# Kernel optimization log

Measured on AMD Instinct MI355X. Metric: run time of the kernel, lower is better.

## Reference

```python
import jax, jax.numpy as jnp
import numpy as np

D_MODEL = 1024
D_STATE = 8          # max(8, 16 // 2)
D_CONV = 4
D_INNER = int(1.5 * D_MODEL)   # expand = max(1.5, 2*0.75)
DT_RANK = (D_MODEL + 15) // 16 # 64
D_FF = 2 * D_MODEL
B, L = 2, 2048


def layer_norm(x, g, b, eps=1e-5):
    mu = jnp.mean(x, -1, keepdims=True)
    var = jnp.var(x, -1, keepdims=True)
    return (x - mu) * jax.lax.rsqrt(var + eps) * g + b


def setup_inputs() -> dict:
    key = jax.random.key(0)
    ks = jax.random.split(key, 12)
    def n(k, shape, scale=0.02):
        return jax.random.normal(k, shape, dtype=jnp.float32) * scale
    return {
        'x': jax.random.normal(ks[0], (B, L, D_MODEL), dtype=jnp.float32),
        'ln1_g': jnp.ones((D_MODEL,), jnp.float32),
        'ln1_b': jnp.zeros((D_MODEL,), jnp.float32),
        'ln2_g': jnp.ones((D_MODEL,), jnp.float32),
        'ln2_b': jnp.zeros((D_MODEL,), jnp.float32),
        'in_proj_w': n(ks[1], (2 * D_INNER, D_MODEL)),
        'conv_w': n(ks[2], (D_INNER, 1, D_CONV), 0.1),
        'conv_b': jnp.zeros((D_INNER,), jnp.float32),
        'x_proj_w': n(ks[3], (DT_RANK + 2 * D_STATE, D_INNER)),
        'dt_proj_w': n(ks[4], (D_INNER, DT_RANK), 0.1),
        'dt_proj_b': n(ks[5], (D_INNER,), 0.1),
        'A_log': jnp.log(jnp.broadcast_to(jnp.arange(1, D_STATE + 1, dtype=jnp.float32), (D_INNER, D_STATE))),
        'D': jnp.ones((D_INNER,), jnp.float32),
        'out_proj_w': n(ks[6], (D_MODEL, D_INNER)),
        'ffn_w1': n(ks[7], (D_FF, D_MODEL)),
        'ffn_b1': jnp.zeros((D_FF,), jnp.float32),
        'ffn_w2': n(ks[8], (D_MODEL, D_FF)),
        'ffn_b2': jnp.zeros((D_MODEL,), jnp.float32),
    }


def mamba(x, in_proj_w, conv_w, conv_b, x_proj_w, dt_proj_w, dt_proj_b, A_log, Dp, out_proj_w):
    # in_proj -> (x, z)
    xz = x @ in_proj_w.T                       # (B, L, 2*d_inner)
    xi, z = jnp.split(xz, 2, axis=-1)
    # depthwise causal conv over seq, kernel 4
    xc = jnp.transpose(xi, (0, 2, 1))          # (B, d_inner, L)
    xc = jax.lax.conv_general_dilated(
        xc, conv_w, window_strides=(1,), padding=[(D_CONV - 1, 0)],
        dimension_numbers=('NCH', 'OIH', 'NCH'), feature_group_count=D_INNER)
    xc = xc + conv_b[None, :, None]
    u = jax.nn.silu(jnp.transpose(xc, (0, 2, 1)))  # (B, L, d_inner)
    # x_proj -> dt, B, C
    x_dbl = u @ x_proj_w.T
    dt = x_dbl[..., :DT_RANK]
    Bm = x_dbl[..., DT_RANK:DT_RANK + D_STATE]
    Cm = x_dbl[..., DT_RANK + D_STATE:]
    delta = jax.nn.softplus(dt @ dt_proj_w.T + dt_proj_b)  # (B, L, d_inner)
    A = -jnp.exp(A_log)                                    # (d_inner, d_state)
    dA = jnp.exp(jnp.einsum('bld,dn->bldn', delta, A))     # (B, L, d_inner, d_state)
    dBu = jnp.einsum('bld,bln,bld->bldn', delta, Bm, u)
    # selective scan over time
    def step(h, inputs):
        dA_t, dBu_t, C_t = inputs
        h = dA_t * h + dBu_t                   # (B, d_inner, d_state)
        y = jnp.einsum('bdn,bn->bd', h, C_t)
        return h, y
    h0 = jnp.zeros((x.shape[0], D_INNER, D_STATE), x.dtype)
    _, ys = jax.lax.scan(step, h0, (jnp.moveaxis(dA, 1, 0), jnp.moveaxis(dBu, 1, 0), jnp.moveaxis(Cm, 1, 0)))
    y = jnp.moveaxis(ys, 0, 1) + u * Dp        # skip connection D*u
    y = y * jax.nn.silu(z)                     # gate
    return y @ out_proj_w.T


def reference(x, ln1_g, ln1_b, ln2_g, ln2_b, in_proj_w, conv_w, conv_b, x_proj_w,
              dt_proj_w, dt_proj_b, A_log, D, out_proj_w, ffn_w1, ffn_b1, ffn_w2, ffn_b2):
    residual = x
    xp = layer_norm(x, ln1_g, ln1_b)
    x = mamba(xp, in_proj_w, conv_w, conv_b, x_proj_w, dt_proj_w, dt_proj_b, A_log, D, out_proj_w) + residual
    xn = layer_norm(x, ln2_g, ln2_b)
    h = jax.nn.gelu(xn @ ffn_w1.T + ffn_b1, approximate=False)  # dropout is identity in eval
    return x + (h @ ffn_w2.T + ffn_b2)
```

## Files before the change

### kernel.cpp

```cpp
#include <hip/hip_runtime.h>
#include <math.h>

#define D_MODEL 1024
#define D_STATE 8
#define D_CONV  4
#define D_INNER 1536
#define DT_RANK 64
#define D_FF    2048
#define BATCH   2
#define SEQ     2048
#define NROWS   (BATCH*SEQ)
#define NC      32
#define LC      (SEQ/NC)
#define XPAD    128

typedef short bf16x8 __attribute__((ext_vector_type(8)));
typedef unsigned short u16x8 __attribute__((ext_vector_type(8)));
typedef float f32x4  __attribute__((ext_vector_type(4)));

__device__ inline unsigned short f2bf(float x) {
    union { float f; unsigned u; } v; v.f = x;
    unsigned r = v.u + 0x7fffu + ((v.u >> 16) & 1u);
    return (unsigned short)(r >> 16);
}
__device__ inline float bf2f(unsigned short h) {
    union { unsigned u; float f; } v; v.u = ((unsigned)h) << 16;
    return v.f;
}
__device__ inline float softplus_f(float x) {
    return (x > 20.0f) ? x : log1pf(__expf(x));
}
__device__ inline float gelu_f(float x) {
    return 0.5f * x * (1.0f + erff(x * 0.70710678118654752f));
}
__device__ inline float silu_f(float x) {
    return x / (1.0f + __expf(-x));
}
__device__ inline void gload16(const unsigned short* g, unsigned short* l) {
    typedef unsigned int u32;
    __builtin_amdgcn_global_load_lds(
        (const __attribute__((address_space(1))) u32*)g,
        (__attribute__((address_space(3))) u32*)l, 16, 0, 0);
}

#define PHASE_SYNC_PRE()  do { __builtin_amdgcn_s_barrier(); \
                               asm volatile("s_waitcnt lgkmcnt(0)" ::: "memory"); } while (0)
#define PHASE_SYNC_POST() do { __builtin_amdgcn_s_barrier(); } while (0)

__global__ __launch_bounds__(256) void prep_kernel(
    const float* __restrict__ s0, unsigned short* __restrict__ d0,
    const float* __restrict__ s1, unsigned short* __restrict__ d1,
    const float* __restrict__ s2, unsigned short* __restrict__ d2,
    const float* __restrict__ s3, unsigned short* __restrict__ d3,
    const float* __restrict__ s4, unsigned short* __restrict__ d4,
    const float* __restrict__ xpw, unsigned short* __restrict__ xpd,
    const float* __restrict__ x, const float* __restrict__ g1,
    const float* __restrict__ b1, unsigned short* __restrict__ xout) {
    int b = blockIdx.x;
    if (b < 4400) {
        const float* s; unsigned short* d; int base;
        if      (b < 1536) { s = s0; d = d0; base = b * 2048; }
        else if (b < 1584) { s = s1; d = d1; base = (b - 1536) * 2048; }
        else if (b < 2352) { s = s2; d = d2; base = (b - 1584) * 2048; }
        else if (b < 3376) { s = s3; d = d3; base = (b - 2352) * 2048; }
        else               { s = s4; d = d4; base = (b - 3376) * 2048; }
        int i = base + threadIdx.x * 8;
        float4 v0 = *(const float4*)(s + i);
        float4 v1 = *(const float4*)(s + i + 4);
        ushort4 a, c;
        a.x = f2bf(v0.x); a.y = f2bf(v0.y); a.z = f2bf(v0.z); a.w = f2bf(v0.w);
        c.x = f2bf(v1.x); c.y = f2bf(v1.y); c.z = f2bf(v1.z); c.w = f2bf(v1.w);
        *(ushort4*)(d + i)     = a;
        *(ushort4*)(d + i + 4) = c;
    } else if (b < 4528) {
        int row = b - 4400;
        for (int c = threadIdx.x; c < D_INNER; c += 256)
            xpd[row * D_INNER + c] = (row < 80) ? f2bf(xpw[row * D_INNER + c]) : (unsigned short)0;
    } else {
        __shared__ float sbuf[4];
        int row = b - 4528;
        int t = threadIdx.x;
        float4 v = ((const float4*)(x + (size_t)row * D_MODEL))[t];
        float s = v.x + v.y + v.z + v.w;
        for (int o = 32; o; o >>= 1) s += __shfl_down(s, o, 64);
        if ((t & 63) == 0) sbuf[t >> 6] = s;
        __syncthreads();
        float mu = (sbuf[0] + sbuf[1] + sbuf[2] + sbuf[3]) * (1.0f / D_MODEL);
        __syncthreads();
        float e0 = v.x - mu, e1 = v.y - mu, e2 = v.z - mu, e3 = v.w - mu;
        float q = e0*e0 + e1*e1 + e2*e2 + e3*e3;
        for (int o = 32; o; o >>= 1) q += __shfl_down(q, o, 64);
        if ((t & 63) == 0) sbuf[t >> 6] = q;
        __syncthreads();
        float var = (sbuf[0] + sbuf[1] + sbuf[2] + sbuf[3]) * (1.0f / D_MODEL);
        float rs = rsqrtf(var + 1e-5f);
        float4 gv = ((const float4*)g1)[t];
        float4 bv = ((const float4*)b1)[t];
        ushort4 st;
        st.x = f2bf(e0 * rs * gv.x + bv.x);
        st.y = f2bf(e1 * rs * gv.y + bv.y);
        st.z = f2bf(e2 * rs * gv.z + bv.z);
        st.w = f2bf(e3 * rs * gv.w + bv.w);
        ((ushort4*)(xout + (size_t)row * D_MODEL))[t] = st;
    }
}

__global__ __launch_bounds__(256) void ln_kernel(const float* __restrict__ x,
                                                 const float* __restrict__ g,
                                                 const float* __restrict__ b,
                                                 unsigned short* __restrict__ out) {
    __shared__ float sbuf[4];
    int row = blockIdx.x;
    int t = threadIdx.x;
    float4 v = ((const float4*)(x + (size_t)row * D_MODEL))[t];
    float s = v.x + v.y + v.z + v.w;
    for (int o = 32; o; o >>= 1) s += __shfl_down(s, o, 64);
    if ((t & 63) == 0) sbuf[t >> 6] = s;
    __syncthreads();
    float mu = (sbuf[0] + sbuf[1] + sbuf[2] + sbuf[3]) * (1.0f / D_MODEL);
    __syncthreads();
    float d0 = v.x - mu, d1 = v.y - mu, d2 = v.z - mu, d3 = v.w - mu;
    float q = d0*d0 + d1*d1 + d2*d2 + d3*d3;
    for (int o = 32; o; o >>= 1) q += __shfl_down(q, o, 64);
    if ((t & 63) == 0) sbuf[t >> 6] = q;
    __syncthreads();
    float var = (sbuf[0] + sbuf[1] + sbuf[2] + sbuf[3]) * (1.0f / D_MODEL);
    float rs = rsqrtf(var + 1e-5f);
    float4 gv = ((const float4*)g)[t];
    float4 bv = ((const float4*)b)[t];
    ushort4 st;
    st.x = f2bf(d0 * rs * gv.x + bv.x);
    st.y = f2bf(d1 * rs * gv.y + bv.y);
    st.z = f2bf(d2 * rs * gv.z + bv.z);
    st.w = f2bf(d3 * rs * gv.w + bv.w);
    ((ushort4*)(out + (size_t)row * D_MODEL))[t] = st;
}

#define EPI_F32        0
#define EPI_F32_BF16   1
#define EPI_SOFTPLUS   2
#define EPI_RESID      3
#define EPI_GELU_BF16  4
#define EPI_BIAS_RESID 5
#define EPI_BF16       6
#define EPI_SOFTPLUS_BF16 7

template<int WN, int EPI, int SPLITK>
__global__ __launch_bounds__(512, 2) void gemm8p(
    const unsigned short* __restrict__ A, int lda,
    const unsigned short* __restrict__ Bm, int ldb, int K,
    float* __restrict__ Cf, unsigned short* __restrict__ Cb, int ldc,
    const float* __restrict__ bias,
    const float* __restrict__ resid, int ldr) {
    constexpr int WM = 8 / WN;
    constexpr int BN = WN * 64;
    constexpr int RW = 256 / WM;
    constexpr int CW = 64;
    constexpr int MI = RW / 16;
    constexpr int NI = CW / 16;
    constexpr int MIH = MI / 2, NIH = NI / 2;
    constexpr int ABYTES = 256 * 128;
    constexpr int BBYTES = BN * 128;
    constexpr int BOFF = 2 * ABYTES;
    __shared__ unsigned short lds[(2 * ABYTES + 2 * BBYTES) / 2];

    const int t = threadIdx.x, l = t & 63, w = t >> 6;
    const int wr = w / WN, wc = w % WN;

    const int nx = gridDim.x;
    const int nwg = nx * gridDim.y;
    int bid = blockIdx.y * nx + blockIdx.x;
    int q = nwg >> 3;
    int swz = (bid & 7) * q + (bid >> 3);
    const int m0 = (swz / nx) * 256, n0 = (swz % nx) * BN;
    const int kbase = (SPLITK > 1) ? blockIdx.z * K : 0;

    const int sr = l >> 3;
    const int sj = ((l & 7) * 16) ^ ((l >> 3) << 4);
    const int row_l = w * 8;
    const int row_c = (w >> 2) * 64 + (w & 3) * 8;

    auto STG = [&](int bufbyte, int rowbase, const unsigned short* G, int ldg, int gbase, int kt) {
        unsigned short* dst = (unsigned short*)((char*)lds + bufbyte + rowbase * 128);
        const unsigned short* src = G + (size_t)(gbase + rowbase + sr) * ldg + kbase + kt * 64 + (sj >> 1);
        gload16(src, dst);
    };
    auto S_Ah0 = [&](int b, int kt) {
        if (WN == 4) { STG(b * ABYTES, row_l, A, lda, m0, kt);       STG(b * ABYTES, 128 + row_l, A, lda, m0, kt); }
        else         { STG(b * ABYTES, row_c, A, lda, m0, kt);       STG(b * ABYTES, 128 + row_c, A, lda, m0, kt); }
    };
    auto S_Ah1 = [&](int b, int kt) {
        if (WN == 4) { STG(b * ABYTES, 64 + row_l, A, lda, m0, kt);  STG(b * ABYTES, 192 + row_l, A, lda, m0, kt); }
        else         { STG(b * ABYTES, 32 + row_c, A, lda, m0, kt);  STG(b * ABYTES, 160 + row_c, A, lda, m0, kt); }
    };
    auto S_Bc0 = [&](int b, int kt) {
        if (WN == 4) { STG(BOFF + b * BBYTES, row_c, Bm, ldb, n0, kt); STG(BOFF + b * BBYTES, 128 + row_c, Bm, ldb, n0, kt); }
        else         { STG(BOFF + b * BBYTES, row_c, Bm, ldb, n0, kt); }
    };
    auto S_Bc1 = [&](int b, int kt) {
        if (WN == 4) { STG(BOFF + b * BBYTES, 32 + row_c, Bm, ldb, n0, kt); STG(BOFF + b * BBYTES, 160 + row_c, Bm, ldb, n0, kt); }
        else         { STG(BOFF + b * BBYTES, 32 + row_c, Bm, ldb, n0, kt); }
    };

    auto LD = [&](int bytebase, int row, int kb) -> bf16x8 {
        int o = bytebase + row * 128 + (kb ^ ((row & 7) << 4));
        return *(const bf16x8*)((const char*)lds + o);
    };

    f32x4 acc[MI][NI] = {};
    bf16x8 af[MIH][2], b0v[NIH][2], b1v[NIH][2];

    auto LDA_set = [&](int buf, int qr, auto& dst) {
        #pragma unroll
        for (int mi = 0; mi < MIH; mi++)
            #pragma unroll
            for (int ks = 0; ks < 2; ks++)
                dst[mi][ks] = LD(buf * ABYTES, wr * RW + qr * (RW / 2) + mi * 16 + (l & 15),
                                 ks * 64 + (l >> 4) * 16);
    };
    auto LDB_set = [&](int buf, int qc, auto& dst) {
        #pragma unroll
        for (int ni2 = 0; ni2 < NIH; ni2++)
            #pragma unroll
            for (int ks = 0; ks < 2; ks++)
                dst[ni2][ks] = LD(BOFF + buf * BBYTES, wc * CW + qc * 32 + ni2 * 16 + (l & 15),
                                  ks * 64 + (l >> 4) * 16);
    };
    auto MFMA_Q = [&](int qr, int qc, auto& a_, auto& b_) {
        __builtin_amdgcn_s_setprio(1);
        #pragma unroll
        for (int mi = 0; mi < MIH; mi++)
            #pragma unroll
            for (int ni2 = 0; ni2 < NIH; ni2++)
                #pragma unroll
                for (int ks = 0; ks < 2; ks++)
                    acc[qr * MIH + mi][qc * NIH + ni2] =
                        __builtin_amdgcn_mfma_f32_16x16x32_bf16(a_[mi][ks], b_[ni2][ks],
                                                                acc[qr * MIH + mi][qc * NIH + ni2], 0, 0, 0);
        __builtin_amdgcn_s_setprio(0);
    };
    auto VMW = [&](bool last) {
        if (last)            asm volatile("s_waitcnt vmcnt(0)" ::: "memory");
        else if (WN == 4)    asm volatile("s_waitcnt vmcnt(6)" ::: "memory");
        else                 asm volatile("s_waitcnt vmcnt(5)" ::: "memory");
    };

    const int ni_ = K >> 7;

    S_Ah0(0, 0); S_Ah1(0, 0); S_Bc0(0, 0); S_Bc1(0, 0);
    S_Ah0(1, 1); S_Ah1(1, 1); S_Bc0(1, 1); S_Bc1(1, 1);
    if (WN == 4) asm volatile("s_waitcnt vmcnt(8)" ::: "memory");
    else         asm volatile("s_waitcnt vmcnt(6)" ::: "memory");
    __builtin_amdgcn_s_barrier();

    for (int i = 0; i < ni_; i++) {
        const bool last = (i == ni_ - 1);
        const int t2 = 2 * i + 2, t3 = 2 * i + 3;
        LDA_set(0, 0, af); LDB_set(0, 0, b0v);
        if (i) S_Bc0(1, 2 * i + 1);
        PHASE_SYNC_PRE(); MFMA_Q(0, 0, af, b0v); PHASE_SYNC_POST();
        LDB_set(0, 1, b1v);
        if (!last) S_Ah0(0, t2);
        PHASE_SYNC_PRE(); MFMA_Q(0, 1, af, b1v); PHASE_SYNC_POST();
        LDA_set(0, 1, af);
        PHASE_SYNC_PRE(); MFMA_Q(1, 1, af, b1v); PHASE_SYNC_POST();
        LDB_set(0, 0, b0v);
        if (!last) { S_Ah1(0, t2); S_Bc1(0, t2); }
        VMW(last);
        PHASE_SYNC_PRE(); MFMA_Q(1, 0, af, b0v); PHASE_SYNC_POST();
        LDA_set(1, 0, af); LDB_set(1, 0, b0v);
        if (!last) S_Bc0(0, t2);
        PHASE_SYNC_PRE(); MFMA_Q(0, 0, af, b0v); PHASE_SYNC_POST();
        LDB_set(1, 1, b1v);
        if (!last) S_Ah0(1, t3);
        PHASE_SYNC_PRE(); MFMA_Q(0, 1, af, b1v); PHASE_SYNC_POST();
        LDA_set(1, 1, af);
        PHASE_SYNC_PRE(); MFMA_Q(1, 1, af, b1v); PHASE_SYNC_POST();
        LDB_set(1, 0, b0v);
        if (!last) { S_Ah1(1, t3); S_Bc1(1, t3); }
        VMW(last);
        PHASE_SYNC_PRE(); MFMA_Q(1, 0, af, b0v); PHASE_SYNC_POST();
    }

    float* Cfp = Cf;
    if (SPLITK > 1) Cfp += (size_t)blockIdx.z * NROWS * ldc;
    #pragma unroll
    for (int ni2 = 0; ni2 < NI; ni2++) {
        int col = n0 + wc * CW + ni2 * 16 + (l & 15);
        float bv = 0.0f;
        if (EPI == EPI_SOFTPLUS || EPI == EPI_GELU_BF16 || EPI == EPI_BIAS_RESID) bv = bias[col];
        #pragma unroll
        for (int mi = 0; mi < MI; mi++) {
            #pragma unroll
            for (int j = 0; j < 4; j++) {
                int row = m0 + wr * RW + mi * 16 + (l >> 4) * 4 + j;
                float v = acc[mi][ni2][j];
                if (EPI == EPI_SOFTPLUS)        v = softplus_f(v + bv);
                else if (EPI == EPI_GELU_BF16)  v = gelu_f(v + bv);
                else if (EPI == EPI_RESID)      v = v + resid[(size_t)row * ldr + col];
                else if (EPI == EPI_BIAS_RESID) v = v + bv + resid[(size_t)row * ldr + col];
                if (EPI == EPI_GELU_BF16 || EPI == EPI_BF16) {
                    Cb[(size_t)row * ldc + col] = f2bf(v);
                } else {
                    Cfp[(size_t)row * ldc + col] = v;
                    if (EPI == EPI_F32_BF16) Cb[(size_t)row * ldc + col] = f2bf(v);
                }
            }
        }
    }
}

__global__ __launch_bounds__(256) void sk2_ln(const float* __restrict__ p,
                                              const float* __restrict__ resid,
                                              const float* __restrict__ g,
                                              const float* __restrict__ b,
                                              float* __restrict__ x2,
                                              unsigned short* __restrict__ xn) {
    __shared__ float sbuf[4];
    int row = blockIdx.x;
    int t = threadIdx.x;
    const size_t seg = (size_t)NROWS * D_MODEL;
    size_t base = (size_t)row * D_MODEL + t * 4;
    float4 a = *(const float4*)(p + base);
    float4 bb = *(const float4*)(p + base + seg);
    float4 r = *(const float4*)(resid + base);
    float4 v;
    v.x = a.x + bb.x + r.x;
    v.y = a.y + bb.y + r.y;
    v.z = a.z + bb.z + r.z;
    v.w = a.w + bb.w + r.w;
    *(float4*)(x2 + base) = v;
    float s = v.x + v.y + v.z + v.w;
    for (int o = 32; o; o >>= 1) s += __shfl_down(s, o, 64);
    if ((t & 63) == 0) sbuf[t >> 6] = s;
    __syncthreads();
    float mu = (sbuf[0] + sbuf[1] + sbuf[2] + sbuf[3]) * (1.0f / D_MODEL);
    __syncthreads();
    float d0 = v.x - mu, d1 = v.y - mu, d2 = v.z - mu, d3 = v.w - mu;
    float qq = d0*d0 + d1*d1 + d2*d2 + d3*d3;
    for (int o = 32; o; o >>= 1) qq += __shfl_down(qq, o, 64);
    if ((t & 63) == 0) sbuf[t >> 6] = qq;
    __syncthreads();
    float var = (sbuf[0] + sbuf[1] + sbuf[2] + sbuf[3]) * (1.0f / D_MODEL);
    float rs = rsqrtf(var + 1e-5f);
    float4 gv = ((const float4*)g)[t];
    float4 bv = ((const float4*)b)[t];
    ushort4 st;
    st.x = f2bf(d0 * rs * gv.x + bv.x);
    st.y = f2bf(d1 * rs * gv.y + bv.y);
    st.z = f2bf(d2 * rs * gv.z + bv.z);
    st.w = f2bf(d3 * rs * gv.w + bv.w);
    ((ushort4*)(xn + (size_t)row * D_MODEL))[t] = st;
}

__global__ __launch_bounds__(256) void sk2_reduce(const float* __restrict__ p,
                                                  const float* __restrict__ bias,
                                                  const float* __restrict__ resid,
                                                  float* __restrict__ o) {
    int i = (blockIdx.x * 256 + threadIdx.x) * 4;
    const size_t seg = (size_t)NROWS * D_MODEL;
    float4 a = *(const float4*)(p + i);
    float4 b = *(const float4*)(p + i + seg);
    float4 r = *(const float4*)(resid + i);
    float4 bb = *(const float4*)(bias + (i & (D_MODEL - 1)));
    float4 o4;
    o4.x = a.x + b.x + r.x + bb.x;
    o4.y = a.y + b.y + r.y + bb.y;
    o4.z = a.z + b.z + r.z + bb.z;
    o4.w = a.w + b.w + r.w + bb.w;
    *(float4*)(o + i) = o4;
}

template<int EPI, int SPLITK>
__global__ __launch_bounds__(256) void gemm_mfma(
    const unsigned short* __restrict__ A, int lda,
    const unsigned short* __restrict__ B, int ldb, int K,
    float* __restrict__ Cf, unsigned short* __restrict__ Cb, int ldc,
    const float* __restrict__ bias,
    const float* __restrict__ resid, int ldr) {
    __shared__ unsigned short As[3][128 * 32];
    __shared__ unsigned short Bs[3][128 * 32];
    int t = threadIdx.x, l = t & 63, w = t >> 6;
    int nx = gridDim.x;
    int nwg = nx * gridDim.y;
    int bid = blockIdx.y * nx + blockIdx.x;
    int q = nwg >> 3;
    int swz = (bid & 7) * q + (bid >> 3);
    int m0 = (swz / nx) * 128, n0 = (swz % nx) * 128;
    int kbase = (SPLITK > 1) ? blockIdx.z * K : 0;
    int c0 = 2 * w, c1 = 2 * w + 1;
    int srow = l >> 2, scol = (l & 3) * 8;
    const unsigned short* Ag0 = A + (size_t)(m0 + 16 * c0 + srow) * lda + kbase + scol;
    const unsigned short* Ag1 = A + (size_t)(m0 + 16 * c1 + srow) * lda + kbase + scol;
    const unsigned short* Bg0 = B + (size_t)(n0 + 16 * c0 + srow) * ldb + kbase + scol;
    const unsigned short* Bg1 = B + (size_t)(n0 + 16 * c1 + srow) * ldb + kbase + scol;
    int wr = w >> 1, wc = w & 1;
    int aoff = (wr * 64 + (l & 15)) * 32 + (l >> 4) * 8;
    int boff = (wc * 64 + (l & 15)) * 32 + (l >> 4) * 8;

    f32x4 acc[4][4] = {};
    int nt = K >> 5;

    gload16(Ag0, &As[0][c0 * 512]);
    gload16(Ag1, &As[0][c1 * 512]);
    gload16(Bg0, &Bs[0][c0 * 512]);
    gload16(Bg1, &Bs[0][c1 * 512]);
    if (nt > 1) {
        gload16(Ag0 + 32, &As[1][c0 * 512]);
        gload16(Ag1 + 32, &As[1][c1 * 512]);
        gload16(Bg0 + 32, &Bs[1][c0 * 512]);
        gload16(Bg1 + 32, &Bs[1][c1 * 512]);
    }

    int cur = 0;
    for (int ti = 0; ti < nt; ti++) {
        int pf = ti + 2;
        if (pf < nt) {
            int nb = cur - 1; if (nb < 0) nb += 3;
            int k0 = pf << 5;
            gload16(Ag0 + k0, &As[nb][c0 * 512]);
            gload16(Ag1 + k0, &As[nb][c1 * 512]);
            gload16(Bg0 + k0, &Bs[nb][c0 * 512]);
            gload16(Bg1 + k0, &Bs[nb][c1 * 512]);
        }
        int rem = nt - 1 - ti;
        if (rem >= 2)      asm volatile("s_waitcnt vmcnt(8)" ::: "memory");
        else if (rem == 1) asm volatile("s_waitcnt vmcnt(4)" ::: "memory");
        else               asm volatile("s_waitcnt vmcnt(0)" ::: "memory");
        __builtin_amdgcn_s_barrier();

        const unsigned short* Ab = &As[cur][0];
        const unsigned short* Bb = &Bs[cur][0];
        bf16x8 af[4], bfv[4];
        #pragma unroll
        for (int i = 0; i < 4; i++) af[i] = *(const bf16x8*)(Ab + aoff + i * 512);
        #pragma unroll
        for (int i = 0; i < 4; i++) bfv[i] = *(const bf16x8*)(Bb + boff + i * 512);
        __builtin_amdgcn_s_setprio(1);
        #pragma unroll
        for (int mi = 0; mi < 4; mi++)
            #pragma unroll
            for (int ni = 0; ni < 4; ni++)
                acc[mi][ni] = __builtin_amdgcn_mfma_f32_16x16x32_bf16(af[mi], bfv[ni], acc[mi][ni], 0, 0, 0);
        __builtin_amdgcn_s_setprio(0);
        __builtin_amdgcn_s_barrier();
        cur++; if (cur == 3) cur = 0;
    }

    if (SPLITK > 1) Cf += (size_t)blockIdx.z * NROWS * ldc;
    int colb = n0 + wc * 64 + (l & 15);
    int rowb = m0 + wr * 64 + (l >> 4) * 4;
    #pragma unroll
    for (int ni = 0; ni < 4; ni++) {
        int col = colb + ni * 16;
        float bv = 0.0f;
        if (EPI == EPI_SOFTPLUS || EPI == EPI_GELU_BF16 || EPI == EPI_BIAS_RESID || EPI == EPI_SOFTPLUS_BF16) bv = bias[col];
        #pragma unroll
        for (int mi = 0; mi < 4; mi++) {
            #pragma unroll
            for (int j = 0; j < 4; j++) {
                int row = rowb + mi * 16 + j;
                float v = acc[mi][ni][j];
                if (EPI == EPI_SOFTPLUS || EPI == EPI_SOFTPLUS_BF16) v = softplus_f(v + bv);
                else if (EPI == EPI_GELU_BF16)  v = gelu_f(v + bv);
                else if (EPI == EPI_RESID)      v = v + resid[(size_t)row * ldr + col];
                else if (EPI == EPI_BIAS_RESID) v = v + bv + resid[(size_t)row * ldr + col];
                if (EPI == EPI_GELU_BF16 || EPI == EPI_BF16 || EPI == EPI_SOFTPLUS_BF16) {
                    Cb[(size_t)row * ldc + col] = f2bf(v);
                } else {
                    Cf[(size_t)row * ldc + col] = v;
                    if (EPI == EPI_F32_BF16) Cb[(size_t)row * ldc + col] = f2bf(v);
                }
            }
        }
    }
}

__global__ __launch_bounds__(256) void xdbl_reduce(const float* __restrict__ part,
                                                   float* __restrict__ xdbl,
                                                   unsigned short* __restrict__ xdbl_bf) {
    int i = blockIdx.x * 256 + threadIdx.x;
    const size_t seg = (size_t)NROWS * XPAD;
    float s = part[i] + part[i + seg] + part[i + 2 * seg] + part[i + 3 * seg];
    xdbl[i] = s;
    xdbl_bf[i] = f2bf(s);
}

__global__ __launch_bounds__(256) void conv_silu(const unsigned short* __restrict__ xz,
                                                 const float* __restrict__ w,
                                                 const float* __restrict__ cb,
                                                 unsigned short* __restrict__ u) {
    int idx = (blockIdx.x * 256 + threadIdx.x) * 8;
    int d = idx % D_INNER;
    int bl = idx / D_INNER;
    int l = bl & (SEQ - 1);
    float acc[8];
    float4 wv[8];
    #pragma unroll
    for (int j = 0; j < 8; j++) wv[j] = *(const float4*)(w + (d + j) * 4);
    float4 cb0 = *(const float4*)(cb + d);
    float4 cb1 = *(const float4*)(cb + d + 4);
    acc[0] = cb0.x; acc[1] = cb0.y; acc[2] = cb0.z; acc[3] = cb0.w;
    acc[4] = cb1.x; acc[5] = cb1.y; acc[6] = cb1.z; acc[7] = cb1.w;
    #pragma unroll
    for (int k = 0; k < 4; k++) {
        int lp = l - 3 + k;
        if (lp >= 0) {
            u16x8 s = *(const u16x8*)(xz + (size_t)(bl - 3 + k) * (2 * D_INNER) + d);
            #pragma unroll
            for (int j = 0; j < 8; j++) {
                float wk = (k == 0) ? wv[j].x : (k == 1) ? wv[j].y : (k == 2) ? wv[j].z : wv[j].w;
                acc[j] += bf2f((unsigned short)s[j]) * wk;
            }
        }
    }
    u16x8 o;
    #pragma unroll
    for (int j = 0; j < 8; j++) o[j] = f2bf(silu_f(acc[j]));
    *(u16x8*)(u + idx) = o;
}

__global__ __launch_bounds__(256) void scan_passA(const unsigned short* __restrict__ delta,
                                                  const unsigned short* __restrict__ u,
                                                  const float* __restrict__ xdbl,
                                                  const float* __restrict__ A_log,
                                                  float* __restrict__ P,
                                                  float* __restrict__ S) {
    int d = blockIdx.x * 256 + threadIdx.x;
    int c = blockIdx.y, b = blockIdx.z;
    __shared__ float bc[LC][16];
    int base_row = b * SEQ + c * LC;
    for (int e = threadIdx.x; e < LC * 16; e += 256) {
        int lrr = e >> 4, col = e & 15;
        bc[lrr][col] = xdbl[(size_t)(base_row + lrr) * XPAD + DT_RANK + col];
    }
    __syncthreads();
    float Ad[8];
    #pragma unroll
    for (int n = 0; n < 8; n++) Ad[n] = -__expf(A_log[d * 8 + n]);
    float prod[8], hs[8];
    #pragma unroll
    for (int n = 0; n < 8; n++) { prod[n] = 1.0f; hs[n] = 0.0f; }
    for (int lrr = 0; lrr < LC; lrr++) {
        int row = base_row + lrr;
        float dl = bf2f(delta[(size_t)row * D_INNER + d]);
        float uu = bf2f(u[(size_t)row * D_INNER + d]);
        float du = dl * uu;
        #pragma unroll
        for (int n = 0; n < 8; n++) {
            float dA = __expf(dl * Ad[n]);
            prod[n] *= dA;
            hs[n] = dA * hs[n] + du * bc[lrr][n];
        }
    }
    size_t o = ((size_t)((size_t)b * NC + c) * D_INNER + d) * 8;
    #pragma unroll
    for (int n = 0; n < 8; n++) { P[o + n] = prod[n]; S[o + n] = hs[n]; }
}

__global__ __launch_bounds__(256) void scan_passB(const float* __restrict__ P,
                                                  const float* __restrict__ S,
                                                  float* __restrict__ hstart) {
    int tid = blockIdx.x * 256 + threadIdx.x;
    int b = tid / (D_INNER * 8);
    int rem = tid % (D_INNER * 8);
    float h = 0.0f;
    for (int c = 0; c < NC; c++) {
        size_t o = (size_t)(b * NC + c) * (D_INNER * 8) + rem;
        hstart[o] = h;
        h = P[o] * h + S[o];
    }
}

__global__ __launch_bounds__(256) void scan_passC(const unsigned short* __restrict__ delta,
                                                  const unsigned short* __restrict__ u,
                                                  const float* __restrict__ xdbl,
                                                  const float* __restrict__ A_log,
                                                  const float* __restrict__ hstart,
                                                  const unsigned short* __restrict__ xz,
                                                  const float* __restrict__ Dp,
                                                  unsigned short* __restrict__ ygate) {
    int d = blockIdx.x * 256 + threadIdx.x;
    int c = blockIdx.y, b = blockIdx.z;
    __shared__ float bc[LC][16];
    int base_row = b * SEQ + c * LC;
    for (int e = threadIdx.x; e < LC * 16; e += 256) {
        int lrr = e >> 4, col = e & 15;
        bc[lrr][col] = xdbl[(size_t)(base_row + lrr) * XPAD + DT_RANK + col];
    }
    __syncthreads();
    float Ad[8];
    #pragma unroll
    for (int n = 0; n < 8; n++) Ad[n] = -__expf(A_log[d * 8 + n]);
    float h[8];
    size_t ho = ((size_t)((size_t)b * NC + c) * D_INNER + d) * 8;
    #pragma unroll
    for (int n = 0; n < 8; n++) h[n] = hstart[ho + n];
    float Dd = Dp[d];
    for (int lrr = 0; lrr < LC; lrr++) {
        int row = base_row + lrr;
        float dl = bf2f(delta[(size_t)row * D_INNER + d]);
        float uu = bf2f(u[(size_t)row * D_INNER + d]);
        float du = dl * uu;
        float y = 0.0f;
        #pragma unroll
        for (int n = 0; n < 8; n++) {
            float dA = __expf(dl * Ad[n]);
            h[n] = dA * h[n] + du * bc[lrr][n];
            y += h[n] * bc[lrr][8 + n];
        }
        y += uu * Dd;
        float z = bf2f(xz[(size_t)row * (2 * D_INNER) + D_INNER + d]);
        ygate[(size_t)row * D_INNER + d] = f2bf(y * silu_f(z));
    }
}

extern "C" void kernel_launch(void* const* d_in, const int* in_sizes, int n_in,
                              void* d_out, int out_size, void* d_ws, size_t ws_size,
                              hipStream_t stream) {
    const float* x         = (const float*)d_in[0];
    const float* ln1_g     = (const float*)d_in[1];
    const float* ln1_b     = (const float*)d_in[2];
    const float* ln2_g     = (const float*)d_in[3];
    const float* ln2_b     = (const float*)d_in[4];
    const float* in_proj_w = (const float*)d_in[5];
    const float* conv_w    = (const float*)d_in[6];
    const float* conv_b    = (const float*)d_in[7];
    const float* x_proj_w  = (const float*)d_in[8];
    const float* dt_proj_w = (const float*)d_in[9];
    const float* dt_proj_b = (const float*)d_in[10];
    const float* A_log     = (const float*)d_in[11];
    const float* Dp        = (const float*)d_in[12];
    const float* out_proj_w= (const float*)d_in[13];
    const float* ffn_w1    = (const float*)d_in[14];
    const float* ffn_b1    = (const float*)d_in[15];
    const float* ffn_w2    = (const float*)d_in[16];
    const float* ffn_b2    = (const float*)d_in[17];
    float* out = (float*)d_out;

    float* xdbl  = (float*)d_ws;
    float* P     = xdbl + (size_t)NROWS * XPAD;
    float* S     = P + (size_t)BATCH * NC * D_INNER * 8;
    float* hst   = S + (size_t)BATCH * NC * D_INNER * 8;
    float* x2    = hst + (size_t)BATCH * NC * D_INNER * 8;
    float* psum  = x2 + (size_t)NROWS * D_MODEL;
    float* part  = psum;
    unsigned short* xz_bf   = (unsigned short*)(psum + 2 * (size_t)NROWS * D_MODEL);
    unsigned short* xp_bf   = xz_bf + (size_t)NROWS * 2 * D_INNER;
    unsigned short* u_bf    = xp_bf + (size_t)NROWS * D_MODEL;
    unsigned short* xdbl_bf = u_bf + (size_t)NROWS * D_INNER;
    unsigned short* yg_bf   = xdbl_bf + (size_t)NROWS * XPAD;
    unsigned short* dl_bf   = yg_bf + (size_t)NROWS * D_INNER;
    unsigned short* w_in    = dl_bf + (size_t)NROWS * D_INNER;
    unsigned short* w_xp    = w_in + (size_t)2 * D_INNER * D_MODEL;
    unsigned short* w_dt    = w_xp + (size_t)XPAD * D_INNER;
    unsigned short* w_out   = w_dt + (size_t)D_INNER * DT_RANK;
    unsigned short* w_f1    = w_out + (size_t)D_MODEL * D_INNER;
    unsigned short* w_f2    = w_f1 + (size_t)D_FF * D_MODEL;
    unsigned short* hff_bf  = xz_bf;

    prep_kernel<<<4400 + XPAD + NROWS, 256, 0, stream>>>(
        in_proj_w, w_in, dt_proj_w, w_dt, out_proj_w, w_out, ffn_w1, w_f1, ffn_w2, w_f2,
        x_proj_w, w_xp, x, ln1_g, ln1_b, xp_bf);
    gemm8p<4, EPI_BF16, 1><<<dim3(3072 / 256, NROWS / 256), 512, 0, stream>>>(
        xp_bf, D_MODEL, w_in, D_MODEL, D_MODEL, nullptr, xz_bf, 2 * D_INNER, nullptr, nullptr, 0);
    conv_silu<<<(NROWS * D_INNER) / (256 * 8), 256, 0, stream>>>(xz_bf, conv_w, conv_b, u_bf);
    gemm_mfma<EPI_F32, 4><<<dim3(1, NROWS / 128, 4), 256, 0, stream>>>(
        u_bf, D_INNER, w_xp, D_INNER, D_INNER / 4, part, nullptr, XPAD, nullptr, nullptr, 0);
    xdbl_reduce<<<(NROWS * XPAD) / 256, 256, 0, stream>>>(part, xdbl, xdbl_bf);
    gemm_mfma<EPI_SOFTPLUS_BF16, 1><<<dim3(D_INNER / 128, NROWS / 128), 256, 0, stream>>>(
        xdbl_bf, XPAD, w_dt, DT_RANK, DT_RANK, nullptr, dl_bf, D_INNER, dt_proj_b, nullptr, 0);
    scan_passA<<<dim3(D_INNER / 256, NC, BATCH), 256, 0, stream>>>(dl_bf, u_bf, xdbl, A_log, P, S);
    scan_passB<<<(BATCH * D_INNER * 8) / 256, 256, 0, stream>>>(P, S, hst);
    scan_passC<<<dim3(D_INNER / 256, NC, BATCH), 256, 0, stream>>>(dl_bf, u_bf, xdbl, A_log, hst, xz_bf, Dp, yg_bf);
    gemm8p<2, EPI_F32, 2><<<dim3(D_MODEL / 128, NROWS / 256, 2), 512, 0, stream>>>(
        yg_bf, D_INNER, w_out, D_INNER, D_INNER / 2, psum, nullptr, D_MODEL, nullptr, nullptr, 0);
    sk2_ln<<<NROWS, 256, 0, stream>>>(psum, x, ln2_g, ln2_b, x2, xp_bf);
    gemm8p<2, EPI_GELU_BF16, 1><<<dim3(D_FF / 128, NROWS / 256), 512, 0, stream>>>(
        xp_bf, D_MODEL, w_f1, D_MODEL, D_MODEL, nullptr, hff_bf, D_FF, ffn_b1, nullptr, 0);
    gemm8p<2, EPI_F32, 2><<<dim3(D_MODEL / 128, NROWS / 256, 2), 512, 0, stream>>>(
        hff_bf, D_FF, w_f2, D_FF, D_FF / 2, psum, nullptr, D_MODEL, nullptr, nullptr, 0);
    sk2_reduce<<<(NROWS * D_MODEL) / 1024, 256, 0, stream>>>(psum, ffn_b2, x2, out);
}
```

Measured before the change: 281.1 us.

## Fuse conv, x_proj, dt_proj and scan passes into one cooperative kernel

Replaces seven separate launches (conv+silu, split-K x_proj GEMM, reduce, dt_proj GEMM, three scan passes) with one cooperative persistent kernel of 384 blocks that uses grid.sync between stages. The aim is to remove per-launch overhead and tail gaps between small kernels. In exchange, each stage is bound to a fixed block count: the x_proj GEMM runs on only 128 blocks, and grid-wide barriers plus a large shared-memory footprint may limit occupancy.

```diff
diff --git a/kernel.cpp b/kernel.cpp
--- a/kernel.cpp
+++ b/kernel.cpp
@@ -1,5 +1,8 @@
 #include <hip/hip_runtime.h>
+#include <hip/hip_cooperative_groups.h>
 #include <math.h>
+
+namespace cg = cooperative_groups;
 
 #define D_MODEL 1024
 #define D_STATE 8
@@ -13,6 +16,7 @@
 #define NC      32
 #define LC      (SEQ/NC)
 #define XPAD    128
+#define MEGA_BLOCKS 384
 
 typedef short bf16x8 __attribute__((ext_vector_type(8)));
 typedef unsigned short u16x8 __attribute__((ext_vector_type(8)));
@@ -105,37 +109,6 @@
     }
 }
 
-__global__ __launch_bounds__(256) void ln_kernel(const float* __restrict__ x,
-                                                 const float* __restrict__ g,
-                                                 const float* __restrict__ b,
-                                                 unsigned short* __restrict__ out) {
-    __shared__ float sbuf[4];
-    int row = blockIdx.x;
-    int t = threadIdx.x;
-    float4 v = ((const float4*)(x + (size_t)row * D_MODEL))[t];
-    float s = v.x + v.y + v.z + v.w;
-    for (int o = 32; o; o >>= 1) s += __shfl_down(s, o, 64);
-    if ((t & 63) == 0) sbuf[t >> 6] = s;
-    __syncthreads();
-    float mu = (sbuf[0] + sbuf[1] + sbuf[2] + sbuf[3]) * (1.0f / D_MODEL);
-    __syncthreads();
-    float d0 = v.x - mu, d1 = v.y - mu, d2 = v.z - mu, d3 = v.w - mu;
-    float q = d0*d0 + d1*d1 + d2*d2 + d3*d3;
-    for (int o = 32; o; o >>= 1) q += __shfl_down(q, o, 64);
-    if ((t & 63) == 0) sbuf[t >> 6] = q;
-    __syncthreads();
-    float var = (sbuf[0] + sbuf[1] + sbuf[2] + sbuf[3]) * (1.0f / D_MODEL);
-    float rs = rsqrtf(var + 1e-5f);
-    float4 gv = ((const float4*)g)[t];
-    float4 bv = ((const float4*)b)[t];
-    ushort4 st;
-    st.x = f2bf(d0 * rs * gv.x + bv.x);
-    st.y = f2bf(d1 * rs * gv.y + bv.y);
-    st.z = f2bf(d2 * rs * gv.z + bv.z);
-    st.w = f2bf(d3 * rs * gv.w + bv.w);
-    ((ushort4*)(out + (size_t)row * D_MODEL))[t] = st;
-}
-
 #define EPI_F32        0
 #define EPI_F32_BF16   1
 #define EPI_SOFTPLUS   2
@@ -371,23 +344,15 @@
     *(float4*)(o + i) = o4;
 }
 
-template<int EPI, int SPLITK>
-__global__ __launch_bounds__(256) void gemm_mfma(
+template<int EPI>
+__device__ __forceinline__ void gemm128_dev(
     const unsigned short* __restrict__ A, int lda,
-    const unsigned short* __restrict__ B, int ldb, int K,
+    const unsigned short* __restrict__ B, int ldb, int K, int kbase,
+    int m0, int n0,
     float* __restrict__ Cf, unsigned short* __restrict__ Cb, int ldc,
     const float* __restrict__ bias,
-    const float* __restrict__ resid, int ldr) {
-    __shared__ unsigned short As[3][128 * 32];
-    __shared__ unsigned short Bs[3][128 * 32];
+    unsigned short (*As)[128 * 32], unsigned short (*Bs)[128 * 32]) {
     int t = threadIdx.x, l = t & 63, w = t >> 6;
-    int nx = gridDim.x;
-    int nwg = nx * gridDim.y;
-    int bid = blockIdx.y * nx + blockIdx.x;
-    int q = nwg >> 3;
-    int swz = (bid & 7) * q + (bid >> 3);
-    int m0 = (swz / nx) * 128, n0 = (swz % nx) * 128;
-    int kbase = (SPLITK > 1) ? blockIdx.z * K : 0;
     int c0 = 2 * w, c1 = 2 * w + 1;
     int srow = l >> 2, scol = (l & 3) * 8;
     const unsigned short* Ag0 = A + (size_t)(m0 + 16 * c0 + srow) * lda + kbase + scol;
@@ -447,171 +412,193 @@
         cur++; if (cur == 3) cur = 0;
     }
 
-    if (SPLITK > 1) Cf += (size_t)blockIdx.z * NROWS * ldc;
     int colb = n0 + wc * 64 + (l & 15);
     int rowb = m0 + wr * 64 + (l >> 4) * 4;
     #pragma unroll
     for (int ni = 0; ni < 4; ni++) {
         int col = colb + ni * 16;
         float bv = 0.0f;
-        if (EPI == EPI_SOFTPLUS || EPI == EPI_GELU_BF16 || EPI == EPI_BIAS_RESID || EPI == EPI_SOFTPLUS_BF16) bv = bias[col];
+        if (EPI == EPI_SOFTPLUS_BF16) bv = bias[col];
         #pragma unroll
         for (int mi = 0; mi < 4; mi++) {
             #pragma unroll
             for (int j = 0; j < 4; j++) {
                 int row = rowb + mi * 16 + j;
                 float v = acc[mi][ni][j];
-                if (EPI == EPI_SOFTPLUS || EPI == EPI_SOFTPLUS_BF16) v = softplus_f(v + bv);
-                else if (EPI == EPI_GELU_BF16)  v = gelu_f(v + bv);
-                else if (EPI == EPI_RESID)      v = v + resid[(size_t)row * ldr + col];
-                else if (EPI == EPI_BIAS_RESID) v = v + bv + resid[(size_t)row * ldr + col];
-                if (EPI == EPI_GELU_BF16 || EPI == EPI_BF16 || EPI == EPI_SOFTPLUS_BF16) {
+                if (EPI == EPI_SOFTPLUS_BF16) v = softplus_f(v + bv);
+                if (EPI == EPI_SOFTPLUS_BF16) {
                     Cb[(size_t)row * ldc + col] = f2bf(v);
                 } else {
                     Cf[(size_t)row * ldc + col] = v;
-                    if (EPI == EPI_F32_BF16) Cb[(size_t)row * ldc + col] = f2bf(v);
                 }
             }
         }
     }
 }
 
-__global__ __launch_bounds__(256) void xdbl_reduce(const float* __restrict__ part,
-                                                   float* __restrict__ xdbl,
-                                                   unsigned short* __restrict__ xdbl_bf) {
-    int i = blockIdx.x * 256 + threadIdx.x;
-    const size_t seg = (size_t)NROWS * XPAD;
-    float s = part[i] + part[i + seg] + part[i + 2 * seg] + part[i + 3 * seg];
-    xdbl[i] = s;
-    xdbl_bf[i] = f2bf(s);
-}
-
-__global__ __launch_bounds__(256) void conv_silu(const unsigned short* __restrict__ xz,
-                                                 const float* __restrict__ w,
-                                                 const float* __restrict__ cb,
-                                                 unsigned short* __restrict__ u) {
-    int idx = (blockIdx.x * 256 + threadIdx.x) * 8;
-    int d = idx % D_INNER;
-    int bl = idx / D_INNER;
-    int l = bl & (SEQ - 1);
-    float acc[8];
-    float4 wv[8];
-    #pragma unroll
-    for (int j = 0; j < 8; j++) wv[j] = *(const float4*)(w + (d + j) * 4);
-    float4 cb0 = *(const float4*)(cb + d);
-    float4 cb1 = *(const float4*)(cb + d + 4);
-    acc[0] = cb0.x; acc[1] = cb0.y; acc[2] = cb0.z; acc[3] = cb0.w;
-    acc[4] = cb1.x; acc[5] = cb1.y; acc[6] = cb1.z; acc[7] = cb1.w;
-    #pragma unroll
-    for (int k = 0; k < 4; k++) {
-        int lp = l - 3 + k;
-        if (lp >= 0) {
-            u16x8 s = *(const u16x8*)(xz + (size_t)(bl - 3 + k) * (2 * D_INNER) + d);
-            #pragma unroll
-            for (int j = 0; j < 8; j++) {
-                float wk = (k == 0) ? wv[j].x : (k == 1) ? wv[j].y : (k == 2) ? wv[j].z : wv[j].w;
-                acc[j] += bf2f((unsigned short)s[j]) * wk;
+struct MegaArgs {
+    const unsigned short* xz_bf;
+    const float* conv_w; const float* conv_b;
+    unsigned short* u_bf;
+    const unsigned short* w_xp;
+    float* part;
+    float* xdbl; unsigned short* xdbl_bf;
+    const unsigned short* w_dt;
+    const float* dt_b;
+    unsigned short* dl_bf;
+    const float* A_log;
+    float* P; float* S; float* hst;
+    const float* Dp;
+    unsigned short* yg_bf;
+};
+
+__global__ __launch_bounds__(256, 2) void mega_kernel(MegaArgs a) {
+    __shared__ unsigned short As[3][128 * 32];
+    __shared__ unsigned short Bs[3][128 * 32];
+    __shared__ float bc[LC][16];
+    cg::grid_group grid = cg::this_grid();
+    const int bid = blockIdx.x, tid = threadIdx.x;
+
+    for (int i = bid * 256 + tid; i < (NROWS * D_INNER) / 8; i += MEGA_BLOCKS * 256) {
+        int idx = i * 8;
+        int d = idx % D_INNER;
+        int bl = idx / D_INNER;
+        int lq = bl & (SEQ - 1);
+        float av[8];
+        float4 wv[8];
+        #pragma unroll
+        for (int j = 0; j < 8; j++) wv[j] = *(const float4*)(a.conv_w + (d + j) * 4);
+        float4 cb0 = *(const float4*)(a.conv_b + d);
+        float4 cb1 = *(const float4*)(a.conv_b + d + 4);
+        av[0] = cb0.x; av[1] = cb0.y; av[2] = cb0.z; av[3] = cb0.w;
+        av[4] = cb1.x; av[5] = cb1.y; av[6] = cb1.z; av[7] = cb1.w;
+        #pragma unroll
+        for (int k = 0; k < 4; k++) {
+            int lp = lq - 3 + k;
+            if (lp >= 0) {
+                u16x8 s = *(const u16x8*)(a.xz_bf + (size_t)(bl - 3 + k) * (2 * D_INNER) + d);
+                #pragma unroll
+                for (int j = 0; j < 8; j++) {
+                    float wk = (k == 0) ? wv[j].x : (k == 1) ? wv[j].y : (k == 2) ? wv[j].z : wv[j].w;
+                    av[j] += bf2f((unsigned short)s[j]) * wk;
+                }
             }
         }
-    }
-    u16x8 o;
-    #pragma unroll
-    for (int j = 0; j < 8; j++) o[j] = f2bf(silu_f(acc[j]));
-    *(u16x8*)(u + idx) = o;
-}
-
-__global__ __launch_bounds__(256) void scan_passA(const unsigned short* __restrict__ delta,
-                                                  const unsigned short* __restrict__ u,
-                                                  const float* __restrict__ xdbl,
-                                                  const float* __restrict__ A_log,
-                                                  float* __restrict__ P,
-                                                  float* __restrict__ S) {
-    int d = blockIdx.x * 256 + threadIdx.x;
-    int c = blockIdx.y, b = blockIdx.z;
-    __shared__ float bc[LC][16];
-    int base_row = b * SEQ + c * LC;
-    for (int e = threadIdx.x; e < LC * 16; e += 256) {
-        int lrr = e >> 4, col = e & 15;
-        bc[lrr][col] = xdbl[(size_t)(base_row + lrr) * XPAD + DT_RANK + col];
-    }
-    __syncthreads();
-    float Ad[8];
-    #pragma unroll
-    for (int n = 0; n < 8; n++) Ad[n] = -__expf(A_log[d * 8 + n]);
-    float prod[8], hs[8];
-    #pragma unroll
-    for (int n = 0; n < 8; n++) { prod[n] = 1.0f; hs[n] = 0.0f; }
-    for (int lrr = 0; lrr < LC; lrr++) {
-        int row = base_row + lrr;
-        float dl = bf2f(delta[(size_t)row * D_INNER + d]);
-        float uu = bf2f(u[(size_t)row * D_INNER + d]);
-        float du = dl * uu;
-        #pragma unroll
-        for (int n = 0; n < 8; n++) {
-            float dA = __expf(dl * Ad[n]);
-            prod[n] *= dA;
-            hs[n] = dA * hs[n] + du * bc[lrr][n];
-        }
-    }
-    size_t o = ((size_t)((size_t)b * NC + c) * D_INNER + d) * 8;
-    #pragma unroll
-    for (int n = 0; n < 8; n++) { P[o + n] = prod[n]; S[o + n] = hs[n]; }
-}
-
-__global__ __launch_bounds__(256) void scan_passB(const float* __restrict__ P,
-                                                  const float* __restrict__ S,
-                                                  float* __restrict__ hstart) {
-    int tid = blockIdx.x * 256 + threadIdx.x;
-    int b = tid / (D_INNER * 8);
-    int rem = tid % (D_INNER * 8);
-    float h = 0.0f;
-    for (int c = 0; c < NC; c++) {
-        size_t o = (size_t)(b * NC + c) * (D_INNER * 8) + rem;
-        hstart[o] = h;
-        h = P[o] * h + S[o];
-    }
-}
-
-__global__ __launch_bounds__(256) void scan_passC(const unsigned short* __restrict__ delta,
-                                                  const unsigned short* __restrict__ u,
-                                                  const float* __restrict__ xdbl,
-                                                  const float* __restrict__ A_log,
-                                                  const float* __restrict__ hstart,
-                                                  const unsigned short* __restrict__ xz,
-                                                  const float* __restrict__ Dp,
-                                                  unsigned short* __restrict__ ygate) {
-    int d = blockIdx.x * 256 + threadIdx.x;
-    int c = blockIdx.y, b = blockIdx.z;
-    __shared__ float bc[LC][16];
-    int base_row = b * SEQ + c * LC;
-    for (int e = threadIdx.x; e < LC * 16; e += 256) {
-        int lrr = e >> 4, col = e & 15;
-        bc[lrr][col] = xdbl[(size_t)(base_row + lrr) * XPAD + DT_RANK + col];
-    }
-    __syncthreads();
-    float Ad[8];
-    #pragma unroll
-    for (int n = 0; n < 8; n++) Ad[n] = -__expf(A_log[d * 8 + n]);
-    float h[8];
-    size_t ho = ((size_t)((size_t)b * NC + c) * D_INNER + d) * 8;
-    #pragma unroll
-    for (int n = 0; n < 8; n++) h[n] = hstart[ho + n];
-    float Dd = Dp[d];
-    for (int lrr = 0; lrr < LC; lrr++) {
-        int row = base_row + lrr;
-        float dl = bf2f(delta[(size_t)row * D_INNER + d]);
-        float uu = bf2f(u[(size_t)row * D_INNER + d]);
-        float du = dl * uu;
-        float y = 0.0f;
-        #pragma unroll
-        for (int n = 0; n < 8; n++) {
-            float dA = __expf(dl * Ad[n]);
-            h[n] = dA * h[n] + du * bc[lrr][n];
-            y += h[n] * bc[lrr][8 + n];
-        }
-        y += uu * Dd;
-        float z = bf2f(xz[(size_t)row * (2 * D_INNER) + D_INNER + d]);
-        ygate[(size_t)row * D_INNER + d] = f2bf(y * silu_f(z));
+        u16x8 o;
+        #pragma unroll
+        for (int j = 0; j < 8; j++) o[j] = f2bf(silu_f(av[j]));
+        *(u16x8*)(a.u_bf + idx) = o;
+    }
+    __threadfence(); grid.sync();
+
+    if (bid < 128) {
+        int kz = bid >> 5, by = bid & 31;
+        gemm128_dev<EPI_F32>(a.u_bf, D_INNER, a.w_xp, D_INNER, D_INNER / 4, kz * (D_INNER / 4),
+                             by * 128, 0,
+                             a.part + (size_t)kz * NROWS * XPAD, nullptr, XPAD, nullptr, As, Bs);
+    }
+    __threadfence(); grid.sync();
+
+    {
+        const size_t seg = (size_t)NROWS * XPAD;
+        for (int i = bid * 256 + tid; i < NROWS * XPAD; i += MEGA_BLOCKS * 256) {
+            float s = a.part[i] + a.part[i + seg] + a.part[i + 2 * seg] + a.part[i + 3 * seg];
+            a.xdbl[i] = s;
+            a.xdbl_bf[i] = f2bf(s);
+        }
+    }
+    __threadfence(); grid.sync();
+
+    {
+        int bx = bid % 12, by = bid / 12;
+        gemm128_dev<EPI_SOFTPLUS_BF16>(a.xdbl_bf, XPAD, a.w_dt, DT_RANK, DT_RANK, 0,
+                                       by * 128, bx * 128,
+                                       nullptr, a.dl_bf, D_INNER, a.dt_b, As, Bs);
+    }
+    __threadfence(); grid.sync();
+
+    {
+        int d = (bid % 6) * 256 + tid;
+        int c = (bid / 6) % 32, b = bid / 192;
+        int base_row = b * SEQ + c * LC;
+        for (int e = tid; e < LC * 16; e += 256) {
+            int lrr = e >> 4, col = e & 15;
+            bc[lrr][col] = a.xdbl[(size_t)(base_row + lrr) * XPAD + DT_RANK + col];
+        }
+        __syncthreads();
+        float Ad[8];
+        #pragma unroll
+        for (int n = 0; n < 8; n++) Ad[n] = -__expf(a.A_log[d * 8 + n]);
+        float prod[8], hs[8];
+        #pragma unroll
+        for (int n = 0; n < 8; n++) { prod[n] = 1.0f; hs[n] = 0.0f; }
+        for (int lrr = 0; lrr < LC; lrr++) {
+            int row = base_row + lrr;
+            float dl = bf2f(a.dl_bf[(size_t)row * D_INNER + d]);
+            float uu = bf2f(a.u_bf[(size_t)row * D_INNER + d]);
+            float du = dl * uu;
+            #pragma unroll
+            for (int n = 0; n < 8; n++) {
+                float dA = __expf(dl * Ad[n]);
+                prod[n] *= dA;
+                hs[n] = dA * hs[n] + du * bc[lrr][n];
+            }
+        }
+        size_t o = ((size_t)((size_t)b * NC + c) * D_INNER + d) * 8;
+        #pragma unroll
+        for (int n = 0; n < 8; n++) { a.P[o + n] = prod[n]; a.S[o + n] = hs[n]; }
+    }
+    __threadfence(); grid.sync();
+
+    {
+        int tg = bid * 256 + tid;
+        if (tg < BATCH * D_INNER * 8) {
+            int b = tg / (D_INNER * 8);
+            int rem = tg % (D_INNER * 8);
+            float h = 0.0f;
+            for (int c = 0; c < NC; c++) {
+                size_t o = (size_t)(b * NC + c) * (D_INNER * 8) + rem;
+                a.hst[o] = h;
+                h = a.P[o] * h + a.S[o];
+            }
+        }
+    }
+    __threadfence(); grid.sync();
+
+    {
+        int d = (bid % 6) * 256 + tid;
+        int c = (bid / 6) % 32, b = bid / 192;
+        int base_row = b * SEQ + c * LC;
+        __syncthreads();
+        for (int e = tid; e < LC * 16; e += 256) {
+            int lrr = e >> 4, col = e & 15;
+            bc[lrr][col] = a.xdbl[(size_t)(base_row + lrr) * XPAD + DT_RANK + col];
+        }
+        __syncthreads();
+        float Ad[8];
+        #pragma unroll
+        for (int n = 0; n < 8; n++) Ad[n] = -__expf(a.A_log[d * 8 + n]);
+        float h[8];
+        size_t ho = ((size_t)((size_t)b * NC + c) * D_INNER + d) * 8;
+        #pragma unroll
+        for (int n = 0; n < 8; n++) h[n] = a.hst[ho + n];
+        float Dd = a.Dp[d];
+        for (int lrr = 0; lrr < LC; lrr++) {
+            int row = base_row + lrr;
+            float dl = bf2f(a.dl_bf[(size_t)row * D_INNER + d]);
+            float uu = bf2f(a.u_bf[(size_t)row * D_INNER + d]);
+            float du = dl * uu;
+            float y = 0.0f;
+            #pragma unroll
+            for (int n = 0; n < 8; n++) {
+                float dA = __expf(dl * Ad[n]);
+                h[n] = dA * h[n] + du * bc[lrr][n];
+                y += h[n] * bc[lrr][8 + n];
+            }
+            y += uu * Dd;
+            float z = bf2f(a.xz_bf[(size_t)row * (2 * D_INNER) + D_INNER + d]);
+            a.yg_bf[(size_t)row * D_INNER + d] = f2bf(y * silu_f(z));
+        }
     }
 }
 
@@ -664,15 +651,14 @@
         x_proj_w, w_xp, x, ln1_g, ln1_b, xp_bf);
     gemm8p<4, EPI_BF16, 1><<<dim3(3072 / 256, NROWS / 256), 512, 0, stream>>>(
         xp_bf, D_MODEL, w_in, D_MODEL, D_MODEL, nullptr, xz_bf, 2 * D_INNER, nullptr, nullptr, 0);
-    conv_silu<<<(NROWS * D_INNER) / (256 * 8), 256, 0, stream>>>(xz_bf, conv_w, conv_b, u_bf);
-    gemm_mfma<EPI_F32, 4><<<dim3(1, NROWS / 128, 4), 256, 0, stream>>>(
-        u_bf, D_INNER, w_xp, D_INNER, D_INNER / 4, part, nullptr, XPAD, nullptr, nullptr, 0);
-    xdbl_reduce<<<(NROWS * XPAD) / 256, 256, 0, stream>>>(part, xdbl, xdbl_bf);
-    gemm_mfma<EPI_SOFTPLUS_BF16, 1><<<dim3(D_INNER / 128, NROWS / 128), 256, 0, stream>>>(
-        xdbl_bf, XPAD, w_dt, DT_RANK, DT_RANK, nullptr, dl_bf, D_INNER, dt_proj_b, nullptr, 0);
-    scan_passA<<<dim3(D_INNER / 256, NC, BATCH), 256, 0, stream>>>(dl_bf, u_bf, xdbl, A_log, P, S);
-    scan_passB<<<(BATCH * D_INNER * 8) / 256, 256, 0, stream>>>(P, S, hst);
-    scan_passC<<<dim3(D_INNER / 256, NC, BATCH), 256, 0, stream>>>(dl_bf, u_bf, xdbl, A_log, hst, xz_bf, Dp, yg_bf);
+    MegaArgs ma;
+    ma.xz_bf = xz_bf; ma.conv_w = conv_w; ma.conv_b = conv_b; ma.u_bf = u_bf;
+    ma.w_xp = w_xp; ma.part = part; ma.xdbl = xdbl; ma.xdbl_bf = xdbl_bf;
+    ma.w_dt = w_dt; ma.dt_b = dt_proj_b; ma.dl_bf = dl_bf; ma.A_log = A_log;
+    ma.P = P; ma.S = S; ma.hst = hst; ma.Dp = Dp; ma.yg_bf = yg_bf;
+    void* kargs[] = { (void*)&ma };
+    hipLaunchCooperativeKernel(reinterpret_cast<void*>(mega_kernel),
+                               dim3(MEGA_BLOCKS), dim3(256), kargs, 0, stream);
     gemm8p<2, EPI_F32, 2><<<dim3(D_MODEL / 128, NROWS / 256, 2), 512, 0, stream>>>(
         yg_bf, D_INNER, w_out, D_INNER, D_INNER / 2, psum, nullptr, D_MODEL, nullptr, nullptr, 0);
     sk2_ln<<<NROWS, 256, 0, stream>>>(psum, x, ln2_g, ln2_b, x2, xp_bf);
```

Result: slower. 806.6 us (+186.9%).
